# Optimization experiments

Hardware: AMD Instinct MI355X
Metric: run time of the kernel (lower is better)

## Reference

```python
import jax, jax.numpy as jnp
import numpy as np

N, T, F_IN = 20000, 13, 3
E = 320000
NB, NL = 4, 2
C_RES, C_DIL, C_SKIP, C_END = 32, 32, 256, 512
KSZ, KHOP = 2, 4
N_PRED, N_OUT = 12, 2
L = NB * NL
DILS = [2 ** i for _ in range(NB) for i in range(NL)]  # [1,2,1,2,1,2,1,2]
EPS = 1e-5


def _dconv(x, w, d):
    # x: [N,C,T], w: [O,I,K]; valid dilated conv -> [N,O,T-(K-1)*d]
    return jax.lax.conv_general_dilated(x, w, (1,), 'VALID', rhs_dilation=(d,),
                                        dimension_numbers=('NCH', 'OIH', 'NCH'))


def _forward(inputs, edge_src, edge_dst, enter_w, enter_b, filt_w, filt_b, gate_w, gate_b,
             gc_w, gc_b, skip_w, skip_b, bn_g, bn_b, out1_w, out1_b, out2_w, out2_b):
    # inputs: [N,T,F] -> x: [N,C_RES,T] via 1x1 conv (enter)
    x = jnp.einsum('of,ntf->not', enter_w, inputs) + enter_b[None, :, None]
    deg = jax.ops.segment_sum(jnp.ones((E,), x.dtype), edge_dst, num_segments=N)
    deg = jnp.maximum(deg, 1.0)[:, None, None]

    def propagate(h):  # [N,t,C]: mean over incoming edges (normalized diffusion step)
        return jax.ops.segment_sum(h[edge_src], edge_dst, num_segments=N) / deg

    skip = jnp.zeros((N, C_SKIP, T), x.dtype)
    for l in range(L):
        d = DILS[l]
        f = jnp.tanh(_dconv(x, filt_w[l], d) + filt_b[l][None, :, None])
        g = jax.nn.sigmoid(_dconv(x, gate_w[l], d) + gate_b[l][None, :, None])
        h = f * g                                   # [N,C_DIL,t]
        t = h.shape[-1]
        skip = skip[..., -t:] + jnp.einsum('oc,nct->not', skip_w[l], h) + skip_b[l][None, :, None]
        # K-hop graph diffusion conv on [N,t,C]
        hh = h.transpose(0, 2, 1)
        acc = jnp.einsum('ntc,co->nto', hh, gc_w[l, 0])
        cur = hh
        for k in range(1, KHOP):
            cur = propagate(cur)
            acc = acc + jnp.einsum('ntc,co->nto', cur, gc_w[l, k])
        acc = acc + gc_b[l]
        x = acc.transpose(0, 2, 1) + x[..., -t:]    # residual add
        # BatchNorm1d over (N, t) per channel (training-mode batch stats)
        mu = x.mean(axis=(0, 2), keepdims=True)
        var = x.var(axis=(0, 2), keepdims=True)
        x = bn_g[l][None, :, None] * (x - mu) * jax.lax.rsqrt(var + EPS) + bn_b[l][None, :, None]
    y = jax.nn.relu(skip)                           # [N,C_SKIP,1]
    y = jax.nn.relu(jnp.einsum('oc,nct->not', out1_w, y) + out1_b[None, :, None])
    y = jnp.einsum('oc,nct->not', out2_w, y) + out2_b[None, :, None]  # [N,n_pred*n_out,1]
    return y.reshape(N, N_PRED, -1)


def setup_inputs() -> dict:
    key = jax.random.key(0)
    ks = jax.random.split(key, 12)
    s = 0.05
    f32 = jnp.float32
    return {
        'inputs': jax.random.normal(ks[0], (N, T, F_IN), f32),
        'edge_src': jax.random.randint(ks[1], (E,), 0, N),
        'edge_dst': jax.random.randint(ks[2], (E,), 0, N),
        'enter_w': jax.random.normal(ks[3], (C_RES, F_IN), f32) * s,
        'enter_b': jnp.zeros((C_RES,), f32),
        'filt_w': jax.random.normal(ks[4], (L, C_DIL, C_RES, KSZ), f32) * s,
        'filt_b': jnp.zeros((L, C_DIL), f32),
        'gate_w': jax.random.normal(ks[5], (L, C_DIL, C_RES, KSZ), f32) * s,
        'gate_b': jnp.zeros((L, C_DIL), f32),
        'gc_w': jax.random.normal(ks[6], (L, KHOP, C_DIL, C_RES), f32) * s,
        'gc_b': jnp.zeros((L, C_RES), f32),
        'skip_w': jax.random.normal(ks[7], (L, C_SKIP, C_DIL), f32) * s,
        'skip_b': jnp.zeros((L, C_SKIP), f32),
        'bn_g': jnp.ones((L, C_RES), f32),
        'bn_b': jnp.zeros((L, C_RES), f32),
        'out1_w': jax.random.normal(ks[8], (C_END, C_SKIP), f32) * s,
        'out1_b': jnp.zeros((C_END,), f32),
        'out2_w': jax.random.normal(ks[9], (N_PRED * N_OUT, C_END), f32) * s,
        'out2_b': jnp.zeros((N_PRED * N_OUT,), f32),
    }


def reference(inputs, edge_src, edge_dst, enter_w, enter_b, filt_w, filt_b, gate_w, gate_b,
              gc_w, gc_b, skip_w, skip_b, bn_g, bn_b, out1_w, out1_b, out2_w, out2_b):
    return _forward(inputs, edge_src, edge_dst, enter_w, enter_b, filt_w, filt_b, gate_w, gate_b,
                    gc_w, gc_b, skip_w, skip_b, bn_g, bn_b, out1_w, out1_b, out2_w, out2_b)
```

## Files before the change

kernel.cpp:

```cpp
#include <hip/hip_runtime.h>
#include <cmath>

constexpr int N = 20000, T = 13, E = 320000;
constexpr int NB_SCAN = (N + 255) / 256;
constexpr int NPART = 64;
typedef unsigned int uint32;

typedef __attribute__((ext_vector_type(8))) short short8;
typedef __attribute__((ext_vector_type(4))) float f32x4;

__device__ __forceinline__ unsigned short f2bf(float f) {
  unsigned int u = __float_as_uint(f);
  unsigned int r = (u + 0x7FFFu + ((u >> 16) & 1u)) >> 16;
  return (unsigned short)r;
}
__device__ __forceinline__ float bflo(uint32 v) { return __uint_as_float(v << 16); }
__device__ __forceinline__ float bfhi(uint32 v) { return __uint_as_float(v & 0xFFFF0000u); }
__device__ __forceinline__ uint32 packbf(float lo, float hi) {
  return (uint32)f2bf(lo) | ((uint32)f2bf(hi) << 16);
}

constexpr size_t WALIGN = 512;
constexpr size_t align_up(size_t x) { return (x + WALIGN - 1) & ~(WALIGN - 1); }

constexpr size_t XA_OFF  = 0;
constexpr size_t X_SZ    = align_up((size_t)N * 13 * 32 * 4);
constexpr size_t XB_OFF  = XA_OFF + X_SZ;
constexpr size_t H_OFF   = XB_OFF + X_SZ;
constexpr size_t H_SZ    = align_up((size_t)N * 12 * 32 * 4);
constexpr size_t C1_OFF  = H_OFF + H_SZ;
constexpr size_t C2_OFF  = C1_OFF + H_SZ;
constexpr size_t C3_OFF  = C2_OFF + H_SZ;
constexpr size_t HL_OFF  = C3_OFF + H_SZ;
constexpr size_t HL_SZ   = align_up((size_t)N * 256 * 4);
constexpr size_t W2P_OFF = HL_OFF + HL_SZ;
constexpr size_t SB_OFF  = W2P_OFF + align_up(8192 * 4);
constexpr size_t SUMS_OFF = SB_OFF + align_up(256 * 4);
constexpr size_t PAR_OFF  = SUMS_OFF + align_up(8 * NPART * 64 * 4);
constexpr size_t CNT_OFF  = PAR_OFF + align_up(9 * 64 * 4);
constexpr size_t ROW_OFF  = CNT_OFF + align_up((size_t)N * 4);
constexpr size_t FILL_OFF = ROW_OFF + align_up((size_t)(N + 1) * 4);
constexpr size_t COL_OFF  = FILL_OFF + align_up((size_t)N * 4);
constexpr size_t DEG_OFF  = COL_OFF + align_up((size_t)E * 4);
constexpr size_t BP_OFF   = DEG_OFF + align_up((size_t)N * 4);
constexpr size_t CP_OFF   = BP_OFF + align_up(8 * 2048 * 4);
constexpr size_t BW1_OFF  = CP_OFF + align_up(8 * 2176 * 4);
constexpr size_t BW2_OFF  = BW1_OFF + align_up(32768 * 4);
constexpr size_t BS_OFF   = BW2_OFF + align_up(65536 * 4);
constexpr size_t S_OFF  = C2_OFF;

constexpr int SU_CNT1 = 20;
constexpr int SU_SUM1 = SU_CNT1 + 32;
constexpr int SU_OUT1 = SU_SUM1 + 469;
constexpr int SU_PAR1 = SU_OUT1 + 1;
constexpr int SU_GCW1 = SU_PAR1 + 64;
constexpr int SU_BW11 = SU_GCW1 + 128;
constexpr int SU_BW21 = SU_BW11 + 256;
constexpr int SU_W21  = SU_BW21 + 32;
constexpr int SU_SB1  = SU_W21 + 1;
constexpr int SU_CV1  = SU_SB1 + 9;
constexpr int SU_EN1  = SU_CV1 + 16250;

__global__ __launch_bounds__(256) void k_setup(
    const float* __restrict__ inputs, const float* __restrict__ enter_w, const float* __restrict__ enter_b,
    const float* __restrict__ filt_w, const float* __restrict__ filt_b,
    const float* __restrict__ gate_w, const float* __restrict__ gate_b,
    const float* __restrict__ gc_w, const float* __restrict__ skip_w, const float* __restrict__ skip_b,
    const float* __restrict__ out1_w, const float* __restrict__ out2_w,
    int* __restrict__ cnt, float* __restrict__ sums,
    float* __restrict__ dout, int out_sz,
    float* __restrict__ par, uint32* __restrict__ bp, uint32* __restrict__ bw1,
    uint32* __restrict__ bw2, uint32* __restrict__ w2p, float* __restrict__ sbias,
    uint32* __restrict__ cpack, uint32* __restrict__ x) {
  int b = blockIdx.x, tid = threadIdx.x;
  if (b < SU_CNT1) {
    int i = b * 256 + tid;
    if (i < 5000) ((int4*)cnt)[i] = make_int4(0, 0, 0, 0);
  } else if (b < SU_SUM1) {
    int i = (b - SU_CNT1) * 256 + tid;
    if (i < 8192) ((float4*)sums)[i] = make_float4(0.f, 0.f, 0.f, 0.f);
  } else if (b < SU_OUT1) {
    int i = (b - SU_SUM1) * 256 + tid;
    if (i < (out_sz >> 2)) ((float4*)dout)[i] = make_float4(0.f, 0.f, 0.f, 0.f);
  } else if (b < SU_PAR1) {
    if (tid < 64) par[tid] = (tid < 32) ? 1.0f : 0.0f;
  } else if (b < SU_GCW1) {
    int idx = (b - SU_PAR1) * 256 + tid;
    int w4 = idx & 3, lane = (idx >> 2) & 63, hh = (idx >> 8) & 1, s = (idx >> 9) & 3, l = idx >> 11;
    int n = lane & 15, q = lane >> 4;
    int k0 = q * 8 + w4 * 2, o = hh * 16 + n;
    const float* g = gc_w + (((size_t)(l * 4 + s) * 32 + k0) * 32 + o);
    bp[idx] = packbf(g[0], g[32]);
  } else if (b < SU_BW11) {
    int idx = (b - SU_GCW1) * 256 + tid;
    int w4 = idx & 3, lane = (idx >> 2) & 63, ks = (idx >> 8) & 7, ot = idx >> 11;
    int n = lane & 15, q = lane >> 4;
    int c = q * 8 + w4 * 2, o = ot * 16 + n;
    const float* wr = skip_w + ((size_t)ks * 256 + o) * 32 + c;
    bw1[idx] = packbf(wr[0], wr[1]);
  } else if (b < SU_BW21) {
    int idx = (b - SU_BW11) * 256 + tid;
    int w4 = idx & 3, lane = (idx >> 2) & 63, ks = (idx >> 8) & 7, ot = idx >> 11;
    int n = lane & 15, q = lane >> 4;
    int k = ks * 32 + q * 8 + w4 * 2;
    const float* wr = out1_w + (size_t)(ot * 16 + n) * 256 + k;
    bw2[idx] = packbf(wr[0], wr[1]);
  } else if (b < SU_W21) {
    int idx = (b - SU_BW21) * 256 + tid;
    int w4 = idx & 3, lane = (idx >> 2) & 63, ks = (idx >> 8) & 15, ot = idx >> 12;
    int n = lane & 15, q = lane >> 4;
    int k = ks * 32 + q * 8 + w4 * 2;
    int o = ot * 16 + n;
    float v0 = 0.0f, v1 = 0.0f;
    if (o < 24) { const float* wr = out2_w + (size_t)o * 512 + k; v0 = wr[0]; v1 = wr[1]; }
    w2p[idx] = packbf(v0, v1);
  } else if (b < SU_SB1) {
    float s = 0.0f;
    for (int l = 0; l < 8; l++) s += skip_b[l * 256 + tid];
    sbias[tid] = s;
  } else if (b < SU_CV1) {
    int i = (b - SU_SB1) * 256 + tid;
    if (i < 2048) {
      int w4 = i & 3, lane = (i >> 2) & 63, hh = (i >> 8) & 1, ktap = (i >> 9) & 1, sel = i >> 10;
      int n = lane & 15, q = lane >> 4;
      int c0 = q * 8 + w4 * 2, o = hh * 16 + n;
      const float* w = sel ? gate_w : filt_w;
      float v0 = w[((size_t)o * 32 + c0) * 2 + ktap];
      float v1 = w[((size_t)o * 32 + c0 + 1) * 2 + ktap];
      cpack[i] = packbf(v0, v1);
    } else if (i < 2112) {
      int j = i - 2048; int sel = j >> 5; int o = j & 31;
      ((float*)cpack)[2048 + j] = sel ? gate_b[o] : filt_b[o];
    }
  } else {
    int idx = (b - SU_CV1) * 256 + tid;
    int cw = idx & 15; int tmp = idx >> 4; int t = tmp % 13; int n = tmp / 13;
    int c0 = cw * 2;
    const float* ip = inputs + (size_t)n * (13 * 3) + t * 3;
    float v0 = enter_b[c0]     + enter_w[c0 * 3 + 0]       * ip[0] + enter_w[c0 * 3 + 1]       * ip[1] + enter_w[c0 * 3 + 2]       * ip[2];
    float v1 = enter_b[c0 + 1] + enter_w[(c0 + 1) * 3 + 0] * ip[0] + enter_w[(c0 + 1) * 3 + 1] * ip[1] + enter_w[(c0 + 1) * 3 + 2] * ip[2];
    x[idx] = packbf(v0, v1);
  }
}

__global__ void k_count(const int* __restrict__ dst, int* __restrict__ cnt) {
  int i = blockIdx.x * 256 + threadIdx.x;
  if (i < E) atomicAdd(&cnt[dst[i]], 1);
}

__global__ __launch_bounds__(256) void k_scan1(const int* __restrict__ cnt, int* __restrict__ bsum) {
  __shared__ int sc[256];
  int t = threadIdx.x; int idx = blockIdx.x * 256 + t;
  int v = (idx < N) ? cnt[idx] : 0;
  sc[t] = v; __syncthreads();
  for (int off = 1; off < 256; off <<= 1) {
    int u = (t >= off) ? sc[t - off] : 0;
    __syncthreads();
    sc[t] += u;
    __syncthreads();
  }
  if (t == 255) bsum[blockIdx.x] = sc[255];
}

__global__ __launch_bounds__(256) void k_scan3(const int* __restrict__ cnt, const int* __restrict__ bsum,
                                               int* __restrict__ rowptr, int* __restrict__ fill,
                                               float* __restrict__ deginv) {
  __shared__ int sc[256];
  __shared__ int bo[128];
  int t = threadIdx.x; int idx = blockIdx.x * 256 + t;
  if (t < 128) bo[t] = (t < NB_SCAN) ? bsum[t] : 0;
  int v = (idx < N) ? cnt[idx] : 0;
  sc[t] = v; __syncthreads();
  for (int off = 1; off < 128; off <<= 1) {
    int u1 = (t < 128 && t >= off) ? bo[t - off] : 0;
    int u2 = (t >= off) ? sc[t - off] : 0;
    __syncthreads();
    if (t < 128) bo[t] += u1;
    sc[t] += u2;
    __syncthreads();
  }
  {
    int u2 = (t >= 128) ? sc[t - 128] : 0;
    __syncthreads();
    sc[t] += u2;
    __syncthreads();
  }
  if (idx < N) {
    int myoff = bo[blockIdx.x] - bsum[blockIdx.x];
    int run = myoff + sc[t] - v;
    rowptr[idx] = run; fill[idx] = run;
    deginv[idx] = 1.0f / (float)(v > 1 ? v : 1);
  }
  if (blockIdx.x == 0 && t == 0) rowptr[N] = bo[NB_SCAN - 1];
}

__global__ void k_scatter(const int* __restrict__ src, const int* __restrict__ dst,
                          int* __restrict__ fill, int* __restrict__ col) {
  int i = blockIdx.x * 256 + threadIdx.x;
  if (i < E) { int d = dst[i]; int p = atomicAdd(&fill[d], 1); col[p] = src[i]; }
}

template <int TIN, int TOUT, int D, bool LAST>
__global__ __launch_bounds__(256, 4) void k_conv(const uint32* __restrict__ x,
    const uint32* __restrict__ cpbuf, int layer,
    uint32* __restrict__ h, uint32* __restrict__ hlast) {
  constexpr int RS = 34;
  __shared__ float xst[128 * RS];
  int tid = threadIdx.x;
  int wave = tid >> 6, lane = tid & 63;
  int m = lane & 15, q = lane >> 4;
  int nrows = N * TOUT;
  int base = blockIdx.x * 128;

  const uint32* cp = cpbuf + (size_t)layer * 2176;
  short8 bf[2][2][2];
#pragma unroll
  for (int sel = 0; sel < 2; sel++)
#pragma unroll
    for (int kt = 0; kt < 2; kt++)
#pragma unroll
      for (int hh = 0; hh < 2; hh++)
        bf[sel][kt][hh] = *(const short8*)(cp + (size_t)(((sel * 2 + kt) * 2 + hh) * 64 + lane) * 4);
  const float* bias = (const float*)(cp + 2048);
  float fb0 = bias[m], fb1 = bias[16 + m], gb0 = bias[32 + m], gb1 = bias[48 + m];

#pragma unroll
  for (int tile = 0; tile < 2; tile++) {
    int row = base + wave * 32 + tile * 16 + m;
    bool valid = row < nrows;
    int rr = valid ? row : 0;
    int n = rr / TOUT, tt = rr - n * TOUT;
    const uint32* xr = x + ((size_t)n * TIN + tt) * 16 + q * 4;
    short8 a0 = {0,0,0,0,0,0,0,0}, aD = {0,0,0,0,0,0,0,0};
    if (valid) { a0 = *(const short8*)xr; aD = *(const short8*)(xr + D * 16); }
    f32x4 aF0 = {0.f,0.f,0.f,0.f}, aF1 = {0.f,0.f,0.f,0.f};
    f32x4 aG0 = {0.f,0.f,0.f,0.f}, aG1 = {0.f,0.f,0.f,0.f};
    aF0 = __builtin_amdgcn_mfma_f32_16x16x32_bf16(a0, bf[0][0][0], aF0, 0, 0, 0);
    aF0 = __builtin_amdgcn_mfma_f32_16x16x32_bf16(aD, bf[0][1][0], aF0, 0, 0, 0);
    aF1 = __builtin_amdgcn_mfma_f32_16x16x32_bf16(a0, bf[0][0][1], aF1, 0, 0, 0);
    aF1 = __builtin_amdgcn_mfma_f32_16x16x32_bf16(aD, bf[0][1][1], aF1, 0, 0, 0);
    aG0 = __builtin_amdgcn_mfma_f32_16x16x32_bf16(a0, bf[1][0][0], aG0, 0, 0, 0);
    aG0 = __builtin_amdgcn_mfma_f32_16x16x32_bf16(aD, bf[1][1][0], aG0, 0, 0, 0);
    aG1 = __builtin_amdgcn_mfma_f32_16x16x32_bf16(a0, bf[1][0][1], aG1, 0, 0, 0);
    aG1 = __builtin_amdgcn_mfma_f32_16x16x32_bf16(aD, bf[1][1][1], aG1, 0, 0, 0);
#pragma unroll
    for (int r = 0; r < 4; r++) {
      int lrow = wave * 32 + tile * 16 + q * 4 + r;
      float F0 = aF0[r] + fb0, G0 = aG0[r] + gb0;
      float F1 = aF1[r] + fb1, G1 = aG1[r] + gb1;
      float af0 = fabsf(F0), ef0 = __expf(-2.0f * af0);
      float th0 = copysignf((1.0f - ef0) / (1.0f + ef0), F0);
      float hv0 = th0 * (1.0f / (1.0f + __expf(-G0)));
      float af1 = fabsf(F1), ef1 = __expf(-2.0f * af1);
      float th1 = copysignf((1.0f - ef1) / (1.0f + ef1), F1);
      float hv1 = th1 * (1.0f / (1.0f + __expf(-G1)));
      xst[lrow * RS + m]      = hv0;
      xst[lrow * RS + 16 + m] = hv1;
    }
  }
  __syncthreads();
  {
    uint2* outp = (uint2*)h;
#pragma unroll
    for (int it = 0; it < 4; it++) {
      int l = it * 256 + tid;
      int g = base * 8 + l;
      if (g < nrows * 8) {
        int rl = l >> 3, j4 = l & 7;
        float2 a = *(const float2*)&xst[rl * RS + j4 * 4];
        float2 b = *(const float2*)&xst[rl * RS + j4 * 4 + 2];
        uint2 pv = make_uint2(packbf(a.x, a.y), packbf(b.x, b.y));
        if constexpr (!LAST) outp[g] = pv;
        int grow = base + rl;
        int node = grow / TOUT, tt = grow - node * TOUT;
        if (tt == TOUT - 1) {
          *(uint2*)(hlast + (size_t)node * 128 + layer * 16 + j4 * 2) = pv;
        }
      }
    }
  }
}

template <int CH>
__global__ __launch_bounds__(256) void k_hop(const uint32* __restrict__ in, uint32* __restrict__ out,
    const int* __restrict__ rowptr, const int* __restrict__ col, const float* __restrict__ deginv) {
  const uint4* src = (const uint4*)in;
  uint4* dst = (uint4*)out;
  int wid = (blockIdx.x * 256 + threadIdx.x) >> 6;
  int lane = threadIdx.x & 63;
  if (wid >= N) return;
  int s = rowptr[wid], e = rowptr[wid + 1];
  float aL0 = 0.f, aL1 = 0.f, aL2 = 0.f, aL3 = 0.f;
  float aH0 = 0.f, aH1 = 0.f, aH2 = 0.f, aH3 = 0.f;

  if constexpr (CH <= 32) {
    int half = lane >> 5, c = lane & 31;
    bool act = c < CH;
    int idx = s;
    for (; idx + 7 < e; idx += 8) {
      int e0 = col[idx + half], e1 = col[idx + half + 2];
      int e2 = col[idx + half + 4], e3 = col[idx + half + 6];
      if (act) {
        uint4 v0 = src[(size_t)e0 * CH + c];
        uint4 v1 = src[(size_t)e1 * CH + c];
        uint4 v2 = src[(size_t)e2 * CH + c];
        uint4 v3 = src[(size_t)e3 * CH + c];
        aL0 += (bflo(v0.x) + bflo(v1.x)) + (bflo(v2.x) + bflo(v3.x));
        aH0 += (bfhi(v0.x) + bfhi(v1.x)) + (bfhi(v2.x) + bfhi(v3.x));
        aL1 += (bflo(v0.y) + bflo(v1.y)) + (bflo(v2.y) + bflo(v3.y));
        aH1 += (bfhi(v0.y) + bfhi(v1.y)) + (bfhi(v2.y) + bfhi(v3.y));
        aL2 += (bflo(v0.z) + bflo(v1.z)) + (bflo(v2.z) + bflo(v3.z));
        aH2 += (bfhi(v0.z) + bfhi(v1.z)) + (bfhi(v2.z) + bfhi(v3.z));
        aL3 += (bflo(v0.w) + bflo(v1.w)) + (bflo(v2.w) + bflo(v3.w));
        aH3 += (bfhi(v0.w) + bfhi(v1.w)) + (bfhi(v2.w) + bfhi(v3.w));
      }
    }
    for (; idx + 1 < e; idx += 2) {
      int e0 = col[idx + half];
      if (act) {
        uint4 v = src[(size_t)e0 * CH + c];
        aL0 += bflo(v.x); aH0 += bfhi(v.x);
        aL1 += bflo(v.y); aH1 += bfhi(v.y);
        aL2 += bflo(v.z); aH2 += bfhi(v.z);
        aL3 += bflo(v.w); aH3 += bfhi(v.w);
      }
    }
    if (idx < e && half == 0 && act) {
      uint4 v = src[(size_t)col[idx] * CH + c];
      aL0 += bflo(v.x); aH0 += bfhi(v.x);
      aL1 += bflo(v.y); aH1 += bfhi(v.y);
      aL2 += bflo(v.z); aH2 += bfhi(v.z);
      aL3 += bflo(v.w); aH3 += bfhi(v.w);
    }
    aL0 += __shfl_xor(aL0, 32); aH0 += __shfl_xor(aH0, 32);
    aL1 += __shfl_xor(aL1, 32); aH1 += __shfl_xor(aH1, 32);
    aL2 += __shfl_xor(aL2, 32); aH2 += __shfl_xor(aH2, 32);
    aL3 += __shfl_xor(aL3, 32); aH3 += __shfl_xor(aH3, 32);
    float inv = deginv[wid];
    if (half == 0 && act) {
      uint4 o;
      o.x = packbf(aL0 * inv, aH0 * inv);
      o.y = packbf(aL1 * inv, aH1 * inv);
      o.z = packbf(aL2 * inv, aH2 * inv);
      o.w = packbf(aL3 * inv, aH3 * inv);
      dst[(size_t)wid * CH + c] = o;
    }
  } else {
    int c = lane;
    bool act = c < CH;
    int idx = s;
    for (; idx + 3 < e; idx += 4) {
      int e0 = col[idx], e1 = col[idx + 1], e2 = col[idx + 2], e3 = col[idx + 3];
      if (act) {
        uint4 v0 = src[(size_t)e0 * CH + c];
        uint4 v1 = src[(size_t)e1 * CH + c];
        uint4 v2 = src[(size_t)e2 * CH + c];
        uint4 v3 = src[(size_t)e3 * CH + c];
        aL0 += (bflo(v0.x) + bflo(v1.x)) + (bflo(v2.x) + bflo(v3.x));
        aH0 += (bfhi(v0.x) + bfhi(v1.x)) + (bfhi(v2.x) + bfhi(v3.x));
        aL1 += (bflo(v0.y) + bflo(v1.y)) + (bflo(v2.y) + bflo(v3.y));
        aH1 += (bfhi(v0.y) + bfhi(v1.y)) + (bfhi(v2.y) + bfhi(v3.y));
        aL2 += (bflo(v0.z) + bflo(v1.z)) + (bflo(v2.z) + bflo(v3.z));
        aH2 += (bfhi(v0.z) + bfhi(v1.z)) + (bfhi(v2.z) + bfhi(v3.z));
        aL3 += (bflo(v0.w) + bflo(v1.w)) + (bflo(v2.w) + bflo(v3.w));
        aH3 += (bfhi(v0.w) + bfhi(v1.w)) + (bfhi(v2.w) + bfhi(v3.w));
      }
    }
    for (; idx < e; ++idx) {
      int e0 = col[idx];
      if (act) {
        uint4 v = src[(size_t)e0 * CH + c];
        aL0 += bflo(v.x); aH0 += bfhi(v.x);
        aL1 += bflo(v.y); aH1 += bfhi(v.y);
        aL2 += bflo(v.z); aH2 += bfhi(v.z);
        aL3 += bflo(v.w); aH3 += bfhi(v.w);
      }
    }
    float inv = deginv[wid];
    if (act) {
      uint4 o;
      o.x = packbf(aL0 * inv, aH0 * inv);
      o.y = packbf(aL1 * inv, aH1 * inv);
      o.z = packbf(aL2 * inv, aH2 * inv);
      o.w = packbf(aL3 * inv, aH3 * inv);
      dst[(size_t)wid * CH + c] = o;
    }
  }
}

template <int TIN, int TOUT>
__global__ __launch_bounds__(256, 4) void k_combine(const uint32* __restrict__ h,
    const uint32* __restrict__ c1, const uint32* __restrict__ c2, const uint32* __restrict__ c3,
    const uint32* __restrict__ bpack, const float* __restrict__ gcb,
    const uint32* __restrict__ xcur, int layer,
    const float* __restrict__ par,
    uint32* __restrict__ xnext, float* __restrict__ sums) {
  constexpr int RS = 34;
  __shared__ float xst[128 * RS];
  __shared__ float pbuf[96];
  __shared__ float r1s[32], r2s[32];
  int tid = threadIdx.x;
  if (tid < 32) {
    pbuf[tid]      = gcb[layer * 32 + tid];
    pbuf[32 + tid] = par[layer * 64 + tid];
    pbuf[64 + tid] = par[layer * 64 + 32 + tid];
    r1s[tid] = 0.0f; r2s[tid] = 0.0f;
  }

  int nrows = N * TOUT;
  int base = blockIdx.x * 128;
  int wave = tid >> 6, lane = tid & 63;
  int m = lane & 15, q = lane >> 4;

  const uint32* bp = bpack + (size_t)layer * 2048;
  short8 bf[4][2];
#pragma unroll
  for (int s = 0; s < 4; s++)
#pragma unroll
    for (int hh = 0; hh < 2; hh++)
      bf[s][hh] = *(const short8*)(bp + (size_t)((s * 2 + hh) * 64 + lane) * 4);

  f32x4 acc[2][2] = {{{0.f,0.f,0.f,0.f},{0.f,0.f,0.f,0.f}},{{0.f,0.f,0.f,0.f},{0.f,0.f,0.f,0.f}}};
  const uint32* srcs[4] = { h, c1, c2, c3 };
#pragma unroll
  for (int s = 0; s < 4; s++) {
    const uint32* sp = srcs[s];
#pragma unroll
    for (int t = 0; t < 2; t++) {
      int row = base + wave * 32 + t * 16 + m;
      short8 af = {0,0,0,0,0,0,0,0};
      if (row < nrows) af = *(const short8*)(sp + (size_t)row * 16 + q * 4);
      acc[t][0] = __builtin_amdgcn_mfma_f32_16x16x32_bf16(af, bf[s][0], acc[t][0], 0, 0, 0);
      acc[t][1] = __builtin_amdgcn_mfma_f32_16x16x32_bf16(af, bf[s][1], acc[t][1], 0, 0, 0);
    }
  }

  __syncthreads();
#pragma unroll
  for (int t = 0; t < 2; t++)
#pragma unroll
    for (int hh = 0; hh < 2; hh++)
#pragma unroll
      for (int r = 0; r < 4; r++)
        xst[(wave * 32 + t * 16 + q * 4 + r) * RS + hh * 16 + m] = acc[t][hh][r];
  __syncthreads();

  constexpr int toff = TIN - TOUT;
  int rg = tid >> 3, oq = tid & 7;
  float gb0 = pbuf[oq * 4 + 0], gb1 = pbuf[oq * 4 + 1], gb2 = pbuf[oq * 4 + 2], gb3 = pbuf[oq * 4 + 3];
  float sc0 = pbuf[32 + oq * 4 + 0], sc1 = pbuf[32 + oq * 4 + 1], sc2 = pbuf[32 + oq * 4 + 2], sc3 = pbuf[32 + oq * 4 + 3];
  float sh0 = pbuf[64 + oq * 4 + 0], sh1 = pbuf[64 + oq * 4 + 1], sh2 = pbuf[64 + oq * 4 + 2], sh3 = pbuf[64 + oq * 4 + 3];
  float s1[4] = {0.f, 0.f, 0.f, 0.f}, s2[4] = {0.f, 0.f, 0.f, 0.f};
#pragma unroll
  for (int i = 0; i < 4; i++) {
    int r = rg + 32 * i;
    int row = base + r;
    bool act = row < nrows;
    float2 aa = *(const float2*)&xst[r * RS + oq * 4];
    float2 ab = *(const float2*)&xst[r * RS + oq * 4 + 2];
    float xr0 = 0.f, xr1 = 0.f, xr2 = 0.f, xr3 = 0.f;
    if (act) {
      int node = row / TOUT, t_ = row - node * TOUT;
      const uint32* rp = xcur + ((size_t)node * TIN + toff + t_) * 16 + oq * 2;
      uint32 va = rp[0], vb = rp[1];
      xr0 = bflo(va); xr1 = bfhi(va); xr2 = bflo(vb); xr3 = bfhi(vb);
    }
    float v0 = aa.x + gb0 + sc0 * xr0 + sh0;
    float v1 = aa.y + gb1 + sc1 * xr1 + sh1;
    float v2 = ab.x + gb2 + sc2 * xr2 + sh2;
    float v3 = ab.y + gb3 + sc3 * xr3 + sh3;
    *(float2*)&xst[r * RS + oq * 4]     = make_float2(v0, v1);
    *(float2*)&xst[r * RS + oq * 4 + 2] = make_float2(v2, v3);
    if (act) {
      s1[0] += v0; s1[1] += v1; s1[2] += v2; s1[3] += v3;
      s2[0] += v0 * v0; s2[1] += v1 * v1; s2[2] += v2 * v2; s2[3] += v3 * v3;
    }
  }
#pragma unroll
  for (int j = 0; j < 4; j++) {
    atomicAdd(&r1s[oq * 4 + j], s1[j]);
    atomicAdd(&r2s[oq * 4 + j], s2[j]);
  }
  __syncthreads();

  {
    uint2* outp = (uint2*)xnext;
#pragma unroll
    for (int it = 0; it < 4; it++) {
      int l = it * 256 + tid;
      int g = base * 8 + l;
      if (g < nrows * 8) {
        int rl = l >> 3, j4 = l & 7;
        float2 a = *(const float2*)&xst[rl * RS + j4 * 4];
        float2 b = *(const float2*)&xst[rl * RS + j4 * 4 + 2];
        outp[g] = make_uint2(packbf(a.x, a.y), packbf(b.x, b.y));
      }
    }
  }
  {
    int part = blockIdx.x & (NPART - 1);
    float* sp = sums + ((size_t)layer * NPART + part) * 64;
    if (tid < 32) atomicAdd(&sp[tid], r1s[tid]);
    else if (tid < 64) atomicAdd(&sp[tid], r2s[tid - 32]);
  }
}

__global__ __launch_bounds__(256) void k_bnprep(const float* __restrict__ sums,
    const float* __restrict__ bng, const float* __restrict__ bnb, float* __restrict__ par,
    const float* __restrict__ fw, const float* __restrict__ fb,
    const float* __restrict__ gw, const float* __restrict__ gb,
    uint32* __restrict__ cpack, int layer, int tout) {
  __shared__ float red1[8][32];
  __shared__ float red2[8][32];
  __shared__ float pb[64];
  int tid = threadIdx.x;
  {
    int o = tid & 31, grp = tid >> 5;
    float t1 = 0.f, t2 = 0.f;
    const float* lp = sums + (size_t)layer * NPART * 64;
    for (int p = grp; p < NPART; p += 8) {
      t1 += lp[p * 64 + o];
      t2 += lp[p * 64 + 32 + o];
    }
    red1[grp][o] = t1; red2[grp][o] = t2;
  }
  __syncthreads();
  if (tid < 32) {
    float t1 = 0.f, t2 = 0.f;
#pragma unroll
    for (int g = 0; g < 8; g++) { t1 += red1[g][tid]; t2 += red2[g][tid]; }
    float cnt = (float)N * (float)tout;
    float mu = t1 / cnt;
    float var = t2 / cnt - mu * mu;
    float sc = bng[layer * 32 + tid] * rsqrtf(var + 1e-5f);
    float sh = bnb[layer * 32 + tid] - mu * sc;
    par[(layer + 1) * 64 + tid] = sc;
    par[(layer + 1) * 64 + 32 + tid] = sh;
    pb[tid] = sc; pb[32 + tid] = sh;
  }
  __syncthreads();
  int nl = layer + 1;
  uint32* cbase = cpack + (size_t)nl * 2176;
  for (int tix = tid; tix < 2048 + 64; tix += 256) {
    if (tix < 2048) {
      int w4 = tix & 3, lane2 = (tix >> 2) & 63, hh2 = (tix >> 8) & 1, ktap = (tix >> 9) & 1, sel = tix >> 10;
      int n2 = lane2 & 15, q2 = lane2 >> 4;
      int c0 = q2 * 8 + w4 * 2, o = hh2 * 16 + n2;
      const float* w = sel ? gw : fw;
      float v0 = w[(((size_t)nl * 32 + o) * 32 + c0) * 2 + ktap] * pb[c0];
      float v1 = w[(((size_t)nl * 32 + o) * 32 + c0 + 1) * 2 + ktap] * pb[c0 + 1];
      cbase[tix] = packbf(v0, v1);
    } else {
      int i = tix - 2048; int sel = i >> 5; int o = i & 31;
      const float* w = sel ? gw : fw;
      const float* b = sel ? gb : fb;
      float s = b[nl * 32 + o];
      for (int c = 0; c < 32; c++) {
        float sh2 = pb[32 + c];
        s += (w[(((size_t)nl * 32 + o) * 32 + c) * 2 + 0] +
              w[(((size_t)nl * 32 + o) * 32 + c) * 2 + 1]) * sh2;
      }
      ((float*)cbase)[2048 + i] = s;
    }
  }
}

__global__ __launch_bounds__(256) void k_gemm1(const uint32* __restrict__ A,
    const uint32* __restrict__ bp, const float* __restrict__ bias, uint32* __restrict__ Sb) {
  constexpr int RS = 68;
  __shared__ float xst[128 * RS];
  int tid = threadIdx.x;
  int wave = tid >> 6, lane = tid & 63;
  int m = lane & 15, q = lane >> 4;
  int base = blockIdx.x * 128;
  int ot0 = blockIdx.y * 8;

  f32x4 acc[2][8];
#pragma unroll
  for (int t = 0; t < 2; t++)
#pragma unroll
    for (int nt = 0; nt < 8; nt++) acc[t][nt] = (f32x4){0.f, 0.f, 0.f, 0.f};

  int row0 = base + wave * 32 + m;
  int row1 = row0 + 16;
#pragma unroll 1
  for (int ks = 0; ks < 8; ks++) {
    short8 a0 = {0,0,0,0,0,0,0,0}, a1 = {0,0,0,0,0,0,0,0};
    if (row0 < N) a0 = *(const short8*)(A + (size_t)row0 * 128 + ks * 16 + q * 4);
    if (row1 < N) a1 = *(const short8*)(A + (size_t)row1 * 128 + ks * 16 + q * 4);
#pragma unroll
    for (int nt = 0; nt < 8; nt++) {
      short8 b = *(const short8*)(bp + (size_t)(((ot0 + nt) * 8 + ks) * 64 + lane) * 4);
      acc[0][nt] = __builtin_amdgcn_mfma_f32_16x16x32_bf16(a0, b, acc[0][nt], 0, 0, 0);
      acc[1][nt] = __builtin_amdgcn_mfma_f32_16x16x32_bf16(a1, b, acc[1][nt], 0, 0, 0);
    }
  }

#pragma unroll
  for (int half = 0; half < 2; half++) {
    if (half) __syncthreads();
#pragma unroll
    for (int t = 0; t < 2; t++)
#pragma unroll
      for (int nn = 0; nn < 4; nn++) {
        float bv = bias[blockIdx.y * 128 + (half * 4 + nn) * 16 + m];
#pragma unroll
        for (int r = 0; r < 4; r++) {
          float v = acc[t][half * 4 + nn][r] + bv;
          xst[(wave * 32 + t * 16 + q * 4 + r) * RS + nn * 16 + m] = fmaxf(v, 0.0f);
        }
      }
    __syncthreads();
#pragma unroll
    for (int it = 0; it < 8; it++) {
      int l = it * 256 + tid;
      int rl = l >> 4, c4 = l & 15;
      int grow = base + rl;
      if (grow < N) {
        float2 a = *(const float2*)&xst[rl * RS + c4 * 4];
        float2 b = *(const float2*)&xst[rl * RS + c4 * 4 + 2];
        *(uint2*)(Sb + (size_t)grow * 128 + blockIdx.y * 64 + half * 32 + c4 * 2) =
            make_uint2(packbf(a.x, a.y), packbf(b.x, b.y));
      }
    }
  }
}

__global__ __launch_bounds__(256) void k_gemm2f(const uint32* __restrict__ A,
    const uint32* __restrict__ bp, const float* __restrict__ bias,
    const uint32* __restrict__ w2p, const float* __restrict__ b2, float* __restrict__ out) {
  constexpr int RS = 68;
  __shared__ float xst[128 * RS];
  int tid = threadIdx.x;
  int wave = tid >> 6, lane = tid & 63;
  int m = lane & 15, q = lane >> 4;
  int base = blockIdx.x * 128;
  int ot0 = blockIdx.y * 8;

  f32x4 acc[2][8];
#pragma unroll
  for (int t = 0; t < 2; t++)
#pragma unroll
    for (int nt = 0; nt < 8; nt++) acc[t][nt] = (f32x4){0.f, 0.f, 0.f, 0.f};

  int row0 = base + wave * 32 + m;
  int row1 = row0 + 16;
#pragma unroll 1
  for (int ks = 0; ks < 8; ks++) {
    short8 a0 = {0,0,0,0,0,0,0,0}, a1 = {0,0,0,0,0,0,0,0};
    if (row0 < N) a0 = *(const short8*)(A + (size_t)row0 * 128 + ks * 16 + q * 4);
    if (row1 < N) a1 = *(const short8*)(A + (size_t)row1 * 128 + ks * 16 + q * 4);
#pragma unroll
    for (int nt = 0; nt < 8; nt++) {
      short8 b = *(const short8*)(bp + (size_t)(((ot0 + nt) * 8 + ks) * 64 + lane) * 4);
      acc[0][nt] = __builtin_amdgcn_mfma_f32_16x16x32_bf16(a0, b, acc[0][nt], 0, 0, 0);
      acc[1][nt] = __builtin_amdgcn_mfma_f32_16x16x32_bf16(a1, b, acc[1][nt], 0, 0, 0);
    }
  }

  f32x4 acc2[2][2];
#pragma unroll
  for (int t = 0; t < 2; t++)
#pragma unroll
    for (int o2 = 0; o2 < 2; o2++) acc2[t][o2] = (f32x4){0.f, 0.f, 0.f, 0.f};

#pragma unroll
  for (int half = 0; half < 2; half++) {
    if (half) __syncthreads();
#pragma unroll
    for (int t = 0; t < 2; t++)
#pragma unroll
      for (int nn = 0; nn < 4; nn++) {
        float bv = bias[blockIdx.y * 128 + (half * 4 + nn) * 16 + m];
#pragma unroll
        for (int r = 0; r < 4; r++) {
          float v = acc[t][half * 4 + nn][r] + bv;
          xst[(wave * 32 + t * 16 + q * 4 + r) * RS + nn * 16 + m] = fmaxf(v, 0.0f);
        }
      }
    __syncthreads();
#pragma unroll
    for (int kl = 0; kl < 2; kl++) {
      short8 a2[2];
#pragma unroll
      for (int t = 0; t < 2; t++) {
        const float* xp = &xst[(size_t)(wave * 32 + t * 16 + m) * RS + kl * 32 + q * 8];
        float4 f0 = *(const float4*)xp;
        float4 f1 = *(const float4*)(xp + 4);
        uint32 u[4];
        u[0] = packbf(f0.x, f0.y); u[1] = packbf(f0.z, f0.w);
        u[2] = packbf(f1.x, f1.y); u[3] = packbf(f1.z, f1.w);
        a2[t] = *(const short8*)u;
      }
      int ksg = blockIdx.y * 4 + half * 2 + kl;
#pragma unroll
      for (int o2 = 0; o2 < 2; o2++) {
        short8 b = *(const short8*)(w2p + (size_t)(((o2 * 16 + ksg) * 64 + lane) * 4));
        acc2[0][o2] = __builtin_amdgcn_mfma_f32_16x16x32_bf16(a2[0], b, acc2[0][o2], 0, 0, 0);
        acc2[1][o2] = __builtin_amdgcn_mfma_f32_16x16x32_bf16(a2[1], b, acc2[1][o2], 0, 0, 0);
      }
    }
  }

#pragma unroll
  for (int t = 0; t < 2; t++)
#pragma unroll
    for (int o2 = 0; o2 < 2; o2++) {
      int oc = o2 * 16 + m;
      if (oc < 24) {
#pragma unroll
        for (int r = 0; r < 4; r++) {
          int row = base + wave * 32 + t * 16 + q * 4 + r;
          if (row < N) {
            float v = acc2[t][o2][r];
            if (blockIdx.y == 0) v += b2[oc];
            atomicAdd(&out[(size_t)row * 24 + oc], v);
          }
        }
      }
    }
}

struct Ptrs {
  const float *fw, *fb, *gw, *gb, *gcb, *bng, *bnb;
  const uint32 *bpack;
  uint32 *cpack;
  void *H, *C1, *C2, *C3;
  uint32 *HL;
  float *par, *sums;
  const int *row, *col;
  const float *deg;
};

template <int TIN, int TOUT, int D, bool LAST>
static void run_layer(int layer, const Ptrs& P, uint32*& xc, uint32*& xn, hipStream_t stream) {
  int cblocks = (N * TOUT + 127) / 128;
  k_conv<TIN, TOUT, D, LAST><<<cblocks, 256, 0, stream>>>(xc, P.cpack, layer, (uint32*)P.H, P.HL);
  if (!LAST) {
    constexpr int CH = TOUT * 4;
    int hb = (N * 64 + 255) / 256;
    k_hop<CH><<<hb, 256, 0, stream>>>((const uint32*)P.H, (uint32*)P.C1, P.row, P.col, P.deg);
    k_hop<CH><<<hb, 256, 0, stream>>>((const uint32*)P.C1, (uint32*)P.C2, P.row, P.col, P.deg);
    k_hop<CH><<<hb, 256, 0, stream>>>((const uint32*)P.C2, (uint32*)P.C3, P.row, P.col, P.deg);
    k_combine<TIN, TOUT><<<cblocks, 256, 0, stream>>>((const uint32*)P.H, (const uint32*)P.C1,
                                                      (const uint32*)P.C2, (const uint32*)P.C3,
                                                      P.bpack, P.gcb, xc, layer, P.par, xn, P.sums);
    k_bnprep<<<1, 256, 0, stream>>>(P.sums, P.bng, P.bnb, P.par, P.fw, P.fb, P.gw, P.gb,
                                    P.cpack, layer, TOUT);
    uint32* tmp = xc; xc = xn; xn = tmp;
  }
}

extern "C" void kernel_launch(void* const* d_in, const int* in_sizes, int n_in,
                              void* d_out, int out_size, void* d_ws, size_t ws_size,
                              hipStream_t stream) {
  const float* inputs  = (const float*)d_in[0];
  const int*   esrc    = (const int*)d_in[1];
  const int*   edst    = (const int*)d_in[2];
  const float* enter_w = (const float*)d_in[3];
  const float* enter_b = (const float*)d_in[4];
  const float* filt_w  = (const float*)d_in[5];
  const float* filt_b  = (const float*)d_in[6];
  const float* gate_w  = (const float*)d_in[7];
  const float* gate_b  = (const float*)d_in[8];
  const float* gc_w    = (const float*)d_in[9];
  const float* gc_b    = (const float*)d_in[10];
  const float* skip_w  = (const float*)d_in[11];
  const float* skip_b  = (const float*)d_in[12];
  const float* bn_g    = (const float*)d_in[13];
  const float* bn_b    = (const float*)d_in[14];
  const float* out1_w  = (const float*)d_in[15];
  const float* out1_b  = (const float*)d_in[16];
  const float* out2_w  = (const float*)d_in[17];
  const float* out2_b  = (const float*)d_in[18];

  char* ws = (char*)d_ws;
  uint32* XA = (uint32*)(ws + XA_OFF);
  uint32* XB = (uint32*)(ws + XB_OFF);
  void* H    = (void*)(ws + H_OFF);
  void* C1   = (void*)(ws + C1_OFF);
  void* C2   = (void*)(ws + C2_OFF);
  void* C3   = (void*)(ws + C3_OFF);
  uint32* HLB = (uint32*)(ws + HL_OFF);
  uint32* W2P = (uint32*)(ws + W2P_OFF);
  float* SB  = (float*)(ws + SB_OFF);
  float* SUMS = (float*)(ws + SUMS_OFF);
  float* PAR  = (float*)(ws + PAR_OFF);
  int* CNT  = (int*)(ws + CNT_OFF);
  int* ROW  = (int*)(ws + ROW_OFF);
  int* FILL = (int*)(ws + FILL_OFF);
  int* COL  = (int*)(ws + COL_OFF);
  float* DEG = (float*)(ws + DEG_OFF);
  uint32* BP = (uint32*)(ws + BP_OFF);
  uint32* CP = (uint32*)(ws + CP_OFF);
  uint32* BW1 = (uint32*)(ws + BW1_OFF);
  uint32* BW2 = (uint32*)(ws + BW2_OFF);
  int* BS = (int*)(ws + BS_OFF);
  uint32* Sb  = (uint32*)(ws + S_OFF);

  k_setup<<<SU_EN1, 256, 0, stream>>>(inputs, enter_w, enter_b, filt_w, filt_b, gate_w, gate_b,
                                      gc_w, skip_w, skip_b, out1_w, out2_w,
                                      CNT, SUMS, (float*)d_out, out_size,
                                      PAR, BP, BW1, BW2, W2P, SB, CP, XA);

  k_count<<<(E + 255) / 256, 256, 0, stream>>>(edst, CNT);
  k_scan1<<<NB_SCAN, 256, 0, stream>>>(CNT, BS);
  k_scan3<<<NB_SCAN, 256, 0, stream>>>(CNT, BS, ROW, FILL, DEG);
  k_scatter<<<(E + 255) / 256, 256, 0, stream>>>(esrc, edst, FILL, COL);

  Ptrs P;
  P.fw = filt_w; P.fb = filt_b; P.gw = gate_w; P.gb = gate_b;
  P.gcb = gc_b; P.bng = bn_g; P.bnb = bn_b; P.bpack = BP; P.cpack = CP;
  P.H = H; P.C1 = C1; P.C2 = C2; P.C3 = C3; P.HL = HLB; P.par = PAR; P.sums = SUMS;
  P.row = ROW; P.col = COL; P.deg = DEG;

  uint32* xc = XA; uint32* xn = XB;
  run_layer<13, 12, 1, false>(0, P, xc, xn, stream);
  run_layer<12, 10, 2, false>(1, P, xc, xn, stream);
  run_layer<10, 9, 1, false>(2, P, xc, xn, stream);
  run_layer<9, 7, 2, false>(3, P, xc, xn, stream);
  run_layer<7, 6, 1, false>(4, P, xc, xn, stream);
  run_layer<6, 4, 2, false>(5, P, xc, xn, stream);
  run_layer<4, 3, 1, false>(6, P, xc, xn, stream);
  run_layer<3, 1, 2, true>(7, P, xc, xn, stream);

  dim3 g1((N + 127) / 128, 2);
  k_gemm1<<<g1, 256, 0, stream>>>(HLB, BW1, SB, Sb);
  dim3 g2((N + 127) / 128, 4);
  k_gemm2f<<<g2, 256, 0, stream>>>(Sb, BW2, out1_b, W2P, out2_b, (float*)d_out);
}
```

Baseline: 958.5 us.

## Fuse third diffusion hop into combine and fold BN prep into consumers

The third graph-propagation hop is now computed inside the combine kernel via a CSR gather into shared memory, which removes one k_hop launch and the C3 round trip to global memory. The single-block k_bnprep kernel is also removed: every conv and combine block reduces the partial BN sums itself and folds scale and shift into its weights and bias on the fly. This cuts two launches per layer and the serialising single-block step, but it duplicates the BN reduction and weight packing in every block and adds gather latency to combine.

New measurement: 1.186 ms. 23.8% more time.

```diff
diff --git a/kernel.cpp b/kernel.cpp
--- a/kernel.cpp
+++ b/kernel.cpp
@@ -52,26 +52,22 @@
 constexpr int SU_CNT1 = 20;
 constexpr int SU_SUM1 = SU_CNT1 + 32;
 constexpr int SU_OUT1 = SU_SUM1 + 469;
-constexpr int SU_PAR1 = SU_OUT1 + 1;
-constexpr int SU_GCW1 = SU_PAR1 + 64;
+constexpr int SU_GCW1 = SU_OUT1 + 64;
 constexpr int SU_BW11 = SU_GCW1 + 128;
 constexpr int SU_BW21 = SU_BW11 + 256;
 constexpr int SU_W21  = SU_BW21 + 32;
 constexpr int SU_SB1  = SU_W21 + 1;
-constexpr int SU_CV1  = SU_SB1 + 9;
-constexpr int SU_EN1  = SU_CV1 + 16250;
+constexpr int SU_EN1  = SU_SB1 + 16250;
 
 __global__ __launch_bounds__(256) void k_setup(
     const float* __restrict__ inputs, const float* __restrict__ enter_w, const float* __restrict__ enter_b,
-    const float* __restrict__ filt_w, const float* __restrict__ filt_b,
-    const float* __restrict__ gate_w, const float* __restrict__ gate_b,
     const float* __restrict__ gc_w, const float* __restrict__ skip_w, const float* __restrict__ skip_b,
     const float* __restrict__ out1_w, const float* __restrict__ out2_w,
     int* __restrict__ cnt, float* __restrict__ sums,
     float* __restrict__ dout, int out_sz,
-    float* __restrict__ par, uint32* __restrict__ bp, uint32* __restrict__ bw1,
+    uint32* __restrict__ bp, uint32* __restrict__ bw1,
     uint32* __restrict__ bw2, uint32* __restrict__ w2p, float* __restrict__ sbias,
-    uint32* __restrict__ cpack, uint32* __restrict__ x) {
+    uint32* __restrict__ x) {
   int b = blockIdx.x, tid = threadIdx.x;
   if (b < SU_CNT1) {
     int i = b * 256 + tid;
@@ -82,10 +78,8 @@
   } else if (b < SU_OUT1) {
     int i = (b - SU_SUM1) * 256 + tid;
     if (i < (out_sz >> 2)) ((float4*)dout)[i] = make_float4(0.f, 0.f, 0.f, 0.f);
-  } else if (b < SU_PAR1) {
-    if (tid < 64) par[tid] = (tid < 32) ? 1.0f : 0.0f;
   } else if (b < SU_GCW1) {
-    int idx = (b - SU_PAR1) * 256 + tid;
+    int idx = (b - SU_OUT1) * 256 + tid;
     int w4 = idx & 3, lane = (idx >> 2) & 63, hh = (idx >> 8) & 1, s = (idx >> 9) & 3, l = idx >> 11;
     int n = lane & 15, q = lane >> 4;
     int k0 = q * 8 + w4 * 2, o = hh * 16 + n;
@@ -118,22 +112,8 @@
     float s = 0.0f;
     for (int l = 0; l < 8; l++) s += skip_b[l * 256 + tid];
     sbias[tid] = s;
-  } else if (b < SU_CV1) {
-    int i = (b - SU_SB1) * 256 + tid;
-    if (i < 2048) {
-      int w4 = i & 3, lane = (i >> 2) & 63, hh = (i >> 8) & 1, ktap = (i >> 9) & 1, sel = i >> 10;
-      int n = lane & 15, q = lane >> 4;
-      int c0 = q * 8 + w4 * 2, o = hh * 16 + n;
-      const float* w = sel ? gate_w : filt_w;
-      float v0 = w[((size_t)o * 32 + c0) * 2 + ktap];
-      float v1 = w[((size_t)o * 32 + c0 + 1) * 2 + ktap];
-      cpack[i] = packbf(v0, v1);
-    } else if (i < 2112) {
-      int j = i - 2048; int sel = j >> 5; int o = j & 31;
-      ((float*)cpack)[2048 + j] = sel ? gate_b[o] : filt_b[o];
-    }
   } else {
-    int idx = (b - SU_CV1) * 256 + tid;
+    int idx = (b - SU_SB1) * 256 + tid;
     int cw = idx & 15; int tmp = idx >> 4; int t = tmp % 13; int n = tmp / 13;
     int c0 = cw * 2;
     const float* ip = inputs + (size_t)n * (13 * 3) + t * 3;
@@ -202,27 +182,77 @@
 
 template <int TIN, int TOUT, int D, bool LAST>
 __global__ __launch_bounds__(256, 4) void k_conv(const uint32* __restrict__ x,
-    const uint32* __restrict__ cpbuf, int layer,
+    const float* __restrict__ fw, const float* __restrict__ fb,
+    const float* __restrict__ gw, const float* __restrict__ gb,
+    const float* __restrict__ sums, const float* __restrict__ bng, const float* __restrict__ bnb,
+    int layer,
     uint32* __restrict__ h, uint32* __restrict__ hlast) {
   constexpr int RS = 34;
   __shared__ float xst[128 * RS];
+  __shared__ float pb[64];
+  __shared__ float bias_s[64];
+  __shared__ float red[256];
   int tid = threadIdx.x;
   int wave = tid >> 6, lane = tid & 63;
   int m = lane & 15, q = lane >> 4;
   int nrows = N * TOUT;
   int base = blockIdx.x * 128;
 
-  const uint32* cp = cpbuf + (size_t)layer * 2176;
+  if (layer == 0) {
+    if (tid < 64) pb[tid] = (tid < 32) ? 1.0f : 0.0f;
+  } else {
+    const float* lp = sums + (size_t)(layer - 1) * NPART * 64;
+    int o = tid & 63, grp = tid >> 6;
+    float t1 = 0.f;
+    for (int p = grp; p < NPART; p += 4) t1 += lp[p * 64 + o];
+    red[grp * 64 + o] = t1;
+    __syncthreads();
+    if (tid < 64) red[tid] = red[tid] + red[64 + tid] + red[128 + tid] + red[192 + tid];
+    __syncthreads();
+    if (tid < 32) {
+      float cnt = (float)N * (float)TIN;
+      float mu = red[tid] / cnt;
+      float var = red[32 + tid] / cnt - mu * mu;
+      float sc = bng[(layer - 1) * 32 + tid] * rsqrtf(var + 1e-5f);
+      pb[tid] = sc;
+      pb[32 + tid] = bnb[(layer - 1) * 32 + tid] - mu * sc;
+    }
+  }
+  __syncthreads();
+
+  if (tid < 64) {
+    int sel = tid >> 5, o = tid & 31;
+    const float* w = sel ? gw : fw;
+    const float* b = sel ? gb : fb;
+    const float* wr = w + ((size_t)layer * 32 + o) * 64;
+    float s = b[layer * 32 + o];
+    for (int c = 0; c < 32; c++) s += (wr[c * 2] + wr[c * 2 + 1]) * pb[32 + c];
+    bias_s[tid] = s;
+  }
+
   short8 bf[2][2][2];
 #pragma unroll
-  for (int sel = 0; sel < 2; sel++)
-#pragma unroll
-    for (int kt = 0; kt < 2; kt++)
-#pragma unroll
-      for (int hh = 0; hh < 2; hh++)
-        bf[sel][kt][hh] = *(const short8*)(cp + (size_t)(((sel * 2 + kt) * 2 + hh) * 64 + lane) * 4);
-  const float* bias = (const float*)(cp + 2048);
-  float fb0 = bias[m], fb1 = bias[16 + m], gb0 = bias[32 + m], gb1 = bias[48 + m];
+  for (int sel = 0; sel < 2; sel++) {
+    const float* w = sel ? gw : fw;
+#pragma unroll
+    for (int hh = 0; hh < 2; hh++) {
+      int o = hh * 16 + m;
+      const float* wr = w + ((size_t)layer * 32 + o) * 64;
+      union { uint32 u[4]; short8 s8; } f0, f1;
+#pragma unroll
+      for (int w4 = 0; w4 < 4; w4++) {
+        int c0 = q * 8 + w4 * 2;
+        float4 v = *(const float4*)(wr + c0 * 2);
+        float sc0 = pb[c0], sc1 = pb[c0 + 1];
+        f0.u[w4] = packbf(v.x * sc0, v.z * sc1);
+        f1.u[w4] = packbf(v.y * sc0, v.w * sc1);
+      }
+      bf[sel][0][hh] = f0.s8;
+      bf[sel][1][hh] = f1.s8;
+    }
+  }
+  __syncthreads();
+  float fb0 = bias_s[m], fb1 = bias_s[16 + m], gb0 = bias_s[32 + m], gb1 = bias_s[48 + m];
 
 #pragma unroll
   for (int tile = 0; tile < 2; tile++) {
@@ -390,27 +420,80 @@
 
 template <int TIN, int TOUT>
 __global__ __launch_bounds__(256, 4) void k_combine(const uint32* __restrict__ h,
-    const uint32* __restrict__ c1, const uint32* __restrict__ c2, const uint32* __restrict__ c3,
+    const uint32* __restrict__ c1, const uint32* __restrict__ c2,
     const uint32* __restrict__ bpack, const float* __restrict__ gcb,
     const uint32* __restrict__ xcur, int layer,
-    const float* __restrict__ par,
+    const float* __restrict__ bng, const float* __restrict__ bnb,
+    const int* __restrict__ rowptr, const int* __restrict__ col, const float* __restrict__ deginv,
     uint32* __restrict__ xnext, float* __restrict__ sums) {
   constexpr int RS = 34;
+  constexpr int RS3 = 20;
   __shared__ float xst[128 * RS];
+  __shared__ uint32 c3s[128 * RS3];
   __shared__ float pbuf[96];
+  __shared__ float red[256];
   __shared__ float r1s[32], r2s[32];
   int tid = threadIdx.x;
-  if (tid < 32) {
-    pbuf[tid]      = gcb[layer * 32 + tid];
-    pbuf[32 + tid] = par[layer * 64 + tid];
-    pbuf[64 + tid] = par[layer * 64 + 32 + tid];
-    r1s[tid] = 0.0f; r2s[tid] = 0.0f;
-  }
-
   int nrows = N * TOUT;
   int base = blockIdx.x * 128;
   int wave = tid >> 6, lane = tid & 63;
   int m = lane & 15, q = lane >> 4;
+  if (tid < 32) {
+    pbuf[tid] = gcb[layer * 32 + tid];
+    r1s[tid] = 0.0f; r2s[tid] = 0.0f;
+  }
+
+#pragma unroll
+  for (int it = 0; it < 8; it++) {
+    int item = it * 256 + tid;
+    int r = item >> 4, c = item & 15;
+    int row = base + r;
+    uint32 outv = 0;
+    if (row < nrows) {
+      int node = row / TOUT, t = row - node * TOUT;
+      int s0 = rowptr[node], e0 = rowptr[node + 1];
+      size_t off = (size_t)t * 16 + c;
+      float alo = 0.f, ahi = 0.f;
+      int idx = s0;
+      for (; idx + 3 < e0; idx += 4) {
+        uint32 v0 = c2[(size_t)col[idx]     * (TOUT * 16) + off];
+        uint32 v1 = c2[(size_t)col[idx + 1] * (TOUT * 16) + off];
+        uint32 v2 = c2[(size_t)col[idx + 2] * (TOUT * 16) + off];
+        uint32 v3 = c2[(size_t)col[idx + 3] * (TOUT * 16) + off];
+        alo += (bflo(v0) + bflo(v1)) + (bflo(v2) + bflo(v3));
+        ahi += (bfhi(v0) + bfhi(v1)) + (bfhi(v2) + bfhi(v3));
+      }
+      for (; idx < e0; ++idx) {
+        uint32 v = c2[(size_t)col[idx] * (TOUT * 16) + off];
+        alo += bflo(v); ahi += bfhi(v);
+      }
+      float inv = deginv[node];
+      outv = packbf(alo * inv, ahi * inv);
+    }
+    c3s[r * RS3 + c] = outv;
+  }
+
+  if (layer == 0) {
+    if (tid < 64) pbuf[32 + tid] = (tid < 32) ? 1.0f : 0.0f;
+  } else {
+    const float* lp = sums + (size_t)(layer - 1) * NPART * 64;
+    int o = tid & 63, grp = tid >> 6;
+    float t1 = 0.f;
+    for (int p = grp; p < NPART; p += 4) t1 += lp[p * 64 + o];
+    red[grp * 64 + o] = t1;
+    __syncthreads();
+    if (tid < 64) red[tid] = red[tid] + red[64 + tid] + red[128 + tid] + red[192 + tid];
+    __syncthreads();
+    if (tid < 32) {
+      float cnt = (float)N * (float)TIN;
+      float mu = red[tid] / cnt;
+      float var = red[32 + tid] / cnt - mu * mu;
+      float sc = bng[(layer - 1) * 32 + tid] * rsqrtf(var + 1e-5f);
+      pbuf[32 + tid] = sc;
+      pbuf[64 + tid] = bnb[(layer - 1) * 32 + tid] - mu * sc;
+    }
+  }
+  __syncthreads();
 
   const uint32* bp = bpack + (size_t)layer * 2048;
   short8 bf[4][2];
@@ -421,15 +504,18 @@
       bf[s][hh] = *(const short8*)(bp + (size_t)((s * 2 + hh) * 64 + lane) * 4);
 
   f32x4 acc[2][2] = {{{0.f,0.f,0.f,0.f},{0.f,0.f,0.f,0.f}},{{0.f,0.f,0.f,0.f},{0.f,0.f,0.f,0.f}}};
-  const uint32* srcs[4] = { h, c1, c2, c3 };
+  const uint32* srcs[3] = { h, c1, c2 };
 #pragma unroll
   for (int s = 0; s < 4; s++) {
-    const uint32* sp = srcs[s];
 #pragma unroll
     for (int t = 0; t < 2; t++) {
       int row = base + wave * 32 + t * 16 + m;
       short8 af = {0,0,0,0,0,0,0,0};
-      if (row < nrows) af = *(const short8*)(sp + (size_t)row * 16 + q * 4);
+      if (s < 3) {
+        if (row < nrows) af = *(const short8*)(srcs[s] + (size_t)row * 16 + q * 4);
+      } else {
+        af = *(const short8*)&c3s[(wave * 32 + t * 16 + m) * RS3 + q * 4];
+      }
       acc[t][0] = __builtin_amdgcn_mfma_f32_16x16x32_bf16(af, bf[s][0], acc[t][0], 0, 0, 0);
       acc[t][1] = __builtin_amdgcn_mfma_f32_16x16x32_bf16(af, bf[s][1], acc[t][1], 0, 0, 0);
     }
@@ -505,66 +591,6 @@
   }
 }
 
-__global__ __launch_bounds__(256) void k_bnprep(const float* __restrict__ sums,
-    const float* __restrict__ bng, const float* __restrict__ bnb, float* __restrict__ par,
-    const float* __restrict__ fw, const float* __restrict__ fb,
-    const float* __restrict__ gw, const float* __restrict__ gb,
-    uint32* __restrict__ cpack, int layer, int tout) {
-  __shared__ float red1[8][32];
-  __shared__ float red2[8][32];
-  __shared__ float pb[64];
-  int tid = threadIdx.x;
-  {
-    int o = tid & 31, grp = tid >> 5;
-    float t1 = 0.f, t2 = 0.f;
-    const float* lp = sums + (size_t)layer * NPART * 64;
-    for (int p = grp; p < NPART; p += 8) {
-      t1 += lp[p * 64 + o];
-      t2 += lp[p * 64 + 32 + o];
-    }
-    red1[grp][o] = t1; red2[grp][o] = t2;
-  }
-  __syncthreads();
-  if (tid < 32) {
-    float t1 = 0.f, t2 = 0.f;
-#pragma unroll
-    for (int g = 0; g < 8; g++) { t1 += red1[g][tid]; t2 += red2[g][tid]; }
-    float cnt = (float)N * (float)tout;
-    float mu = t1 / cnt;
-    float var = t2 / cnt - mu * mu;
-    float sc = bng[layer * 32 + tid] * rsqrtf(var + 1e-5f);
-    float sh = bnb[layer * 32 + tid] - mu * sc;
-    par[(layer + 1) * 64 + tid] = sc;
-    par[(layer + 1) * 64 + 32 + tid] = sh;
-    pb[tid] = sc; pb[32 + tid] = sh;
-  }
-  __syncthreads();
-  int nl = layer + 1;
-  uint32* cbase = cpack + (size_t)nl * 2176;
-  for (int tix = tid; tix < 2048 + 64; tix += 256) {
-    if (tix < 2048) {
-      int w4 = tix & 3, lane2 = (tix >> 2) & 63, hh2 = (tix >> 8) & 1, ktap = (tix >> 9) & 1, sel = tix >> 10;
-      int n2 = lane2 & 15, q2 = lane2 >> 4;
-      int c0 = q2 * 8 + w4 * 2, o = hh2 * 16 + n2;
-      const float* w = sel ? gw : fw;
-      float v0 = w[(((size_t)nl * 32 + o) * 32 + c0) * 2 + ktap] * pb[c0];
-      float v1 = w[(((size_t)nl * 32 + o) * 32 + c0 + 1) * 2 + ktap] * pb[c0 + 1];
-      cbase[tix] = packbf(v0, v1);
-    } else {
-      int i = tix - 2048; int sel = i >> 5; int o = i & 31;
-      const float* w = sel ? gw : fw;
-      const float* b = sel ? gb : fb;
-      float s = b[nl * 32 + o];
-      for (int c = 0; c < 32; c++) {
-        float sh2 = pb[32 + c];
-        s += (w[(((size_t)nl * 32 + o) * 32 + c) * 2 + 0] +
-              w[(((size_t)nl * 32 + o) * 32 + c) * 2 + 1]) * sh2;
-      }
-      ((float*)cbase)[2048 + i] = s;
-    }
-  }
-}
-
 __global__ __launch_bounds__(256) void k_gemm1(const uint32* __restrict__ A,
     const uint32* __restrict__ bp, const float* __restrict__ bias, uint32* __restrict__ Sb) {
   constexpr int RS = 68;
@@ -724,10 +750,9 @@
 struct Ptrs {
   const float *fw, *fb, *gw, *gb, *gcb, *bng, *bnb;
   const uint32 *bpack;
-  uint32 *cpack;
-  void *H, *C1, *C2, *C3;
+  void *H, *C1, *C2;
   uint32 *HL;
-  float *par, *sums;
+  float *sums;
   const int *row, *col;
   const float *deg;
 };
@@ -735,18 +760,19 @@
 template <int TIN, int TOUT, int D, bool LAST>
 static void run_layer(int layer, const Ptrs& P, uint32*& xc, uint32*& xn, hipStream_t stream) {
   int cblocks = (N * TOUT + 127) / 128;
-  k_conv<TIN, TOUT, D, LAST><<<cblocks, 256, 0, stream>>>(xc, P.cpack, layer, (uint32*)P.H, P.HL);
+  k_conv<TIN, TOUT, D, LAST><<<cblocks, 256, 0, stream>>>(xc, P.fw, P.fb, P.gw, P.gb,
+                                                          P.sums, P.bng, P.bnb, layer,
+                                                          (uint32*)P.H, P.HL);
   if (!LAST) {
     constexpr int CH = TOUT * 4;
     int hb = (N * 64 + 255) / 256;
     k_hop<CH><<<hb, 256, 0, stream>>>((const uint32*)P.H, (uint32*)P.C1, P.row, P.col, P.deg);
     k_hop<CH><<<hb, 256, 0, stream>>>((const uint32*)P.C1, (uint32*)P.C2, P.row, P.col, P.deg);
-    k_hop<CH><<<hb, 256, 0, stream>>>((const uint32*)P.C2, (uint32*)P.C3, P.row, P.col, P.deg);
     k_combine<TIN, TOUT><<<cblocks, 256, 0, stream>>>((const uint32*)P.H, (const uint32*)P.C1,
-                                                      (const uint32*)P.C2, (const uint32*)P.C3,
-                                                      P.bpack, P.gcb, xc, layer, P.par, xn, P.sums);
-    k_bnprep<<<1, 256, 0, stream>>>(P.sums, P.bng, P.bnb, P.par, P.fw, P.fb, P.gw, P.gb,
-                                    P.cpack, layer, TOUT);
+                                                      (const uint32*)P.C2,
+                                                      P.bpack, P.gcb, xc, layer,
+                                                      P.bng, P.bnb, P.row, P.col, P.deg,
+                                                      xn, P.sums);
     uint32* tmp = xc; xc = xn; xn = tmp;
   }
 }
@@ -780,28 +806,25 @@
   void* H    = (void*)(ws + H_OFF);
   void* C1   = (void*)(ws + C1_OFF);
   void* C2   = (void*)(ws + C2_OFF);
-  void* C3   = (void*)(ws + C3_OFF);
   uint32* HLB = (uint32*)(ws + HL_OFF);
   uint32* W2P = (uint32*)(ws + W2P_OFF);
   float* SB  = (float*)(ws + SB_OFF);
   float* SUMS = (float*)(ws + SUMS_OFF);
-  float* PAR  = (float*)(ws + PAR_OFF);
   int* CNT  = (int*)(ws + CNT_OFF);
   int* ROW  = (int*)(ws + ROW_OFF);
   int* FILL = (int*)(ws + FILL_OFF);
   int* COL  = (int*)(ws + COL_OFF);
   float* DEG = (float*)(ws + DEG_OFF);
   uint32* BP = (uint32*)(ws + BP_OFF);
-  uint32* CP = (uint32*)(ws + CP_OFF);
   uint32* BW1 = (uint32*)(ws + BW1_OFF);
   uint32* BW2 = (uint32*)(ws + BW2_OFF);
   int* BS = (int*)(ws + BS_OFF);
   uint32* Sb  = (uint32*)(ws + S_OFF);
 
-  k_setup<<<SU_EN1, 256, 0, stream>>>(inputs, enter_w, enter_b, filt_w, filt_b, gate_w, gate_b,
+  k_setup<<<SU_EN1, 256, 0, stream>>>(inputs, enter_w, enter_b,
                                       gc_w, skip_w, skip_b, out1_w, out2_w,
                                       CNT, SUMS, (float*)d_out, out_size,
-                                      PAR, BP, BW1, BW2, W2P, SB, CP, XA);
+                                      BP, BW1, BW2, W2P, SB, XA);
 
   k_count<<<(E + 255) / 256, 256, 0, stream>>>(edst, CNT);
   k_scan1<<<NB_SCAN, 256, 0, stream>>>(CNT, BS);
@@ -810,8 +833,8 @@
 
   Ptrs P;
   P.fw = filt_w; P.fb = filt_b; P.gw = gate_w; P.gb = gate_b;
-  P.gcb = gc_b; P.bng = bn_g; P.bnb = bn_b; P.bpack = BP; P.cpack = CP;
-  P.H = H; P.C1 = C1; P.C2 = C2; P.C3 = C3; P.HL = HLB; P.par = PAR; P.sums = SUMS;
+  P.gcb = gc_b; P.bng = bn_g; P.bnb = bn_b; P.bpack = BP;
+  P.H = H; P.C1 = C1; P.C2 = C2; P.HL = HLB; P.sums = SUMS;
   P.row = ROW; P.col = COL; P.deg = DEG;
 
   uint32* xc = XA; uint32* xn = XB;
```
